# Kernel tuning notes

Measured on AMD Instinct MI355X. Metric: run time of the kernel, lower is better.

Reference implementation:

```python
import jax, jax.numpy as jnp
import numpy as np

B, S, D = 4, 1024, 1024
H, DK, DV = 16, 64, 64
EPS = 1e-5

def setup_inputs() -> dict:
    key = jax.random.key(0)
    ks = jax.random.split(key, 13)
    sc = lambda n: 1.0 / np.sqrt(n)
    return {
        "Q": jax.random.normal(ks[0], (B, S, D), jnp.float32),
        "K": jax.random.normal(ks[1], (B, S, D), jnp.float32),
        "V": jax.random.normal(ks[2], (B, S, D), jnp.float32),
        "Wq": jax.random.normal(ks[3], (D, H * DK), jnp.float32) * sc(D),
        "bq": jax.random.normal(ks[4], (H * DK,), jnp.float32) * 0.01,
        "Wk": jax.random.normal(ks[5], (D, H * DK), jnp.float32) * sc(D),
        "bk": jax.random.normal(ks[6], (H * DK,), jnp.float32) * 0.01,
        "Wv": jax.random.normal(ks[7], (D, H * DV), jnp.float32) * sc(D),
        "bv": jax.random.normal(ks[8], (H * DV,), jnp.float32) * 0.01,
        "Wo": jax.random.normal(ks[9], (H * DV, D), jnp.float32) * sc(H * DV),
        "bo": jax.random.normal(ks[10], (D,), jnp.float32) * 0.01,
        "pos_k": jax.random.normal(ks[11], (H * S, DK), jnp.float32) * 0.02,
        "pos_v": jax.random.normal(ks[12], (H * S, DV), jnp.float32) * 0.02,
        "gamma": jnp.ones((D,), jnp.float32),
        "beta": jnp.zeros((D,), jnp.float32),
    }

def reference(Q, K, V, Wq, bq, Wk, bk, Wv, bv, Wo, bo, pos_k, pos_v, gamma, beta):
    b = Q.shape[0]
    # projections + head split: [b, h, s, dk/dv]
    q = (Q @ Wq + bq).reshape(b, S, H, DK).transpose(0, 2, 1, 3)
    k = (K @ Wk + bk).reshape(b, S, H, DK).transpose(0, 2, 1, 3)
    v = (V @ Wv + bv).reshape(b, S, H, DV).transpose(0, 2, 1, 3)
    # pos_ids = arange(H*S).view(1, H, S) -> embedding lookup is just a reshape
    K_pos = pos_k.reshape(1, H, S, DK)
    V_pos = pos_v.reshape(1, H, S, DV)
    scores = jnp.einsum("bhqd,bhkd->bhqk", q, k + K_pos) / np.sqrt(DK).astype(np.float32)
    attn = jax.nn.softmax(scores, axis=-1)
    context = jnp.einsum("bhqk,bhkd->bhqd", attn, v + V_pos)
    context = context.transpose(0, 2, 1, 3).reshape(b, S, H * DV)
    out = context @ Wo + bo + Q  # residual
    mu = jnp.mean(out, axis=-1, keepdims=True)
    var = jnp.var(out, axis=-1, keepdims=True)
    out = (out - mu) * jax.lax.rsqrt(var + EPS) * gamma + beta
    return (out, attn)
```

## Files before the change

### kernel.cpp

```cpp
#include <hip/hip_runtime.h>
#include <cstdint>
#include <cstddef>


typedef __attribute__((ext_vector_type(8))) short short8;
typedef __attribute__((ext_vector_type(4))) short short4v;
typedef __attribute__((ext_vector_type(4))) float f32x4;

typedef __attribute__((address_space(1))) void gl_void;
typedef __attribute__((address_space(3))) void lds_void;

#define MFMA16(a, b, c) __builtin_amdgcn_mfma_f32_16x16x32_bf16(a, b, c, 0, 0, 0)

__device__ __forceinline__ unsigned short f2bf(float f) {
  union { float f; unsigned u; } v; v.f = f;
  unsigned r = v.u + 0x7FFFu + ((v.u >> 16) & 1u);
  return (unsigned short)(r >> 16);
}
__device__ __forceinline__ float bf2f(unsigned short h) {
  union { unsigned u; float f; } v; v.u = ((unsigned)h) << 16;
  return v.f;
}

__global__ __launch_bounds__(256) void transpose_w(
    const float* __restrict__ wq, const float* __restrict__ wk,
    const float* __restrict__ wv, const float* __restrict__ wo,
    unsigned short* __restrict__ wt) {
  __shared__ unsigned short tile[64][68];
  const int z = blockIdx.z;
  const float* W = (z == 0) ? wq : (z == 1) ? wk : (z == 2) ? wv : wo;
  unsigned short* out = wt + (size_t)z * 1048576;
  const int n0 = blockIdx.x * 64, k0 = blockIdx.y * 64;
  const int tr = threadIdx.x >> 4;
  const int tc = (threadIdx.x & 15) * 4;
#pragma unroll
  for (int i = 0; i < 4; ++i) {
    int k = tr + i * 16;
    float4 x = *reinterpret_cast<const float4*>(W + (size_t)(k0 + k) * 1024 + n0 + tc);
    tile[k][tc + 0] = f2bf(x.x); tile[k][tc + 1] = f2bf(x.y);
    tile[k][tc + 2] = f2bf(x.z); tile[k][tc + 3] = f2bf(x.w);
  }
  __syncthreads();
#pragma unroll
  for (int i = 0; i < 4; ++i) {
    int n = tr + i * 16;
    short4v o;
    o[0] = (short)tile[tc + 0][n]; o[1] = (short)tile[tc + 1][n];
    o[2] = (short)tile[tc + 2][n]; o[3] = (short)tile[tc + 3][n];
    *reinterpret_cast<short4v*>(out + (size_t)(n0 + n) * 1024 + k0 + tc) = o;
  }
}

__global__ __launch_bounds__(256) void gemm_qkv(
    const float* __restrict__ Qf, const float* __restrict__ Kf,
    const float* __restrict__ Vf, const unsigned short* __restrict__ wt,
    const float* __restrict__ bq, const float* __restrict__ bk,
    const float* __restrict__ bv, const float* __restrict__ pos_k,
    const float* __restrict__ pos_v, unsigned short* __restrict__ qb,
    unsigned short* __restrict__ kbuf, unsigned short* __restrict__ vT) {
  __shared__ unsigned short lds[8192];
  const int z = blockIdx.z;
  const float* A = (z == 0) ? Qf : (z == 1) ? Kf : Vf;
  const unsigned short* Bt = wt + (size_t)z * 1048576;
  const float* bias = (z == 0) ? bq : (z == 1) ? bk : bv;

  const int tid = threadIdx.x;
  const int lane = tid & 63;
  const int w = tid >> 6;
  const int g = lane >> 4;
  const int lr = lane & 15;
  const int wg = blockIdx.y * 8 + blockIdx.x;
  const int lg = (wg & 7) * 32 + (wg >> 3);
  const int m0 = (lg >> 3) << 7;
  const int n0 = (lg & 7) << 7;
  const int wm = w >> 1, wn = w & 1;

  const int ra0 = tid >> 2, ca = tid & 3;
  const int ra1 = ra0 + 64;
  const int wA0 = ra0 * 64 + ((ca ^ ((ra0 >> 1) & 3)) << 4);
  const int wA1 = ra1 * 64 + ((ca ^ ((ra1 >> 1) & 3)) << 4);
  const float* a0p = A + (size_t)(m0 + ra0) * 1024 + ca * 8;
  const float* a1p = A + (size_t)(m0 + ra1) * 1024 + ca * 8;

  const int c0 = (w << 6) + lane;
  const int r0 = c0 >> 2;
  const int sl0 = (c0 & 3) ^ ((r0 >> 1) & 3);
  const int c1 = c0 + 256;
  const int r1 = c1 >> 2;
  const int sl1 = (c1 & 3) ^ ((r1 >> 1) & 3);
  const size_t gb0 = ((size_t)(n0 + r0) << 10) + (sl0 << 3);
  const size_t gb1 = ((size_t)(n0 + r1) << 10) + (sl1 << 3);
  char* ldsc = (char*)lds;
  lds_void* dstB0 = (lds_void*)(ldsc + 8192 + (w << 10));
  lds_void* dstB1 = (lds_void*)(ldsc + 12288 + (w << 10));

  int offA[4], offB[4];
#pragma unroll
  for (int i = 0; i < 4; ++i) {
    int rt = (wm << 6) + (i << 4) + lr;
    offA[i] = rt * 64 + ((g ^ ((rt >> 1) & 3)) << 4);
    int nt = (wn << 6) + (i << 4) + lr;
    offB[i] = 8192 + nt * 64 + ((g ^ ((nt >> 1) & 3)) << 4);
  }

  f32x4 acc[4][4] = {};

  for (int kt = 0; kt < 32; ++kt) {
    const int kb32 = kt << 5;
    __builtin_amdgcn_global_load_lds((gl_void*)(Bt + gb0 + kb32), dstB0, 16, 0, 0);
    __builtin_amdgcn_global_load_lds((gl_void*)(Bt + gb1 + kb32), dstB1, 16, 0, 0);
    const float4 fa = *reinterpret_cast<const float4*>(a0p + kb32);
    const float4 fb = *reinterpret_cast<const float4*>(a0p + kb32 + 4);
    const float4 fc = *reinterpret_cast<const float4*>(a1p + kb32);
    const float4 fd = *reinterpret_cast<const float4*>(a1p + kb32 + 4);
    short8 pa, pb;
    pa[0] = (short)f2bf(fa.x); pa[1] = (short)f2bf(fa.y);
    pa[2] = (short)f2bf(fa.z); pa[3] = (short)f2bf(fa.w);
    pa[4] = (short)f2bf(fb.x); pa[5] = (short)f2bf(fb.y);
    pa[6] = (short)f2bf(fb.z); pa[7] = (short)f2bf(fb.w);
    pb[0] = (short)f2bf(fc.x); pb[1] = (short)f2bf(fc.y);
    pb[2] = (short)f2bf(fc.z); pb[3] = (short)f2bf(fc.w);
    pb[4] = (short)f2bf(fd.x); pb[5] = (short)f2bf(fd.y);
    pb[6] = (short)f2bf(fd.z); pb[7] = (short)f2bf(fd.w);
    *reinterpret_cast<short8*>(ldsc + wA0) = pa;
    *reinterpret_cast<short8*>(ldsc + wA1) = pb;
    __syncthreads();
    short8 am[4], bn[4];
#pragma unroll
    for (int i = 0; i < 4; ++i) {
      am[i] = *reinterpret_cast<const short8*>(ldsc + offA[i]);
      bn[i] = *reinterpret_cast<const short8*>(ldsc + offB[i]);
    }
#pragma unroll
    for (int i = 0; i < 4; ++i)
#pragma unroll
      for (int j = 0; j < 4; ++j)
        acc[i][j] = MFMA16(am[i], bn[j], acc[i][j]);
    __syncthreads();
  }

#pragma unroll
  for (int i = 0; i < 4; ++i) {
#pragma unroll
    for (int j = 0; j < 4; ++j) {
      const int n = n0 + (wn << 6) + (j << 4) + lr;
      const int hh = n >> 6, dk = n & 63;
      const float bs = bias[n];
      const int mb = m0 + (wm << 6) + (i << 4) + (g << 2);
      const int b = mb >> 10, s0 = mb & 1023;
      if (z == 2) {
        short4v o;
#pragma unroll
        for (int r = 0; r < 4; ++r) {
          const float val = acc[i][j][r] + bs +
                            pos_v[((((size_t)hh << 10) + s0 + r) << 6) + dk];
          o[r] = (short)f2bf(val);
        }
        *reinterpret_cast<short4v*>(
            vT + ((size_t)((b * 16 + hh) * 64 + dk) << 10) + s0) = o;
      } else {
#pragma unroll
        for (int r = 0; r < 4; ++r) {
          float val = acc[i][j][r];
          if (z == 0) {
            val = (val + bs) * 0.125f;
          } else {
            val = val + bs + pos_k[((((size_t)hh << 10) + s0 + r) << 6) + dk];
          }
          unsigned short* dst = (z == 0) ? qb : kbuf;
          dst[((((size_t)(b * 16 + hh) << 10) + s0 + r) << 6) + dk] = f2bf(val);
        }
      }
    }
  }
}

__global__ __launch_bounds__(256) void rowsum_kernel(
    const unsigned short* __restrict__ qb,
    const unsigned short* __restrict__ kb,
    float* __restrict__ l_out) {
  __shared__ char smem[16384];
  const int tid = threadIdx.x;
  const int lane = tid & 63;
  const int w = tid >> 6;
  const int g = lane >> 4;
  const int lr = lane & 15;
  const int wg = ((blockIdx.x & 7) << 7) + (blockIdx.x >> 3);
  const int bh = wg >> 4, qt = wg & 15;
  const int qrow0 = (qt << 6) + (w << 4);
  const size_t headoff = (size_t)bh << 16;

  const size_t qoff = headoff + (size_t)(qrow0 + lr) * 64 + (g << 3);
  const short8 a0 = *reinterpret_cast<const short8*>(qb + qoff);
  const short8 a1 = *reinterpret_cast<const short8*>(qb + qoff + 32);

  const int key0 = tid >> 3, sl0 = (tid & 7) ^ (key0 & 7);
  const int key1 = 32 + (tid >> 3), sl1 = (tid & 7) ^ (key1 & 7);
  const unsigned short* src0 = kb + headoff + (size_t)key0 * 64 + (sl0 << 3);
  const unsigned short* src1 = kb + headoff + (size_t)key1 * 64 + (sl1 << 3);

  float l[4] = {0.f, 0.f, 0.f, 0.f};
  for (int ct = 0; ct < 16; ++ct) {
    const int bo = (ct & 1) << 13;
    const int koff = ct << 12;
    __builtin_amdgcn_global_load_lds((gl_void*)(src0 + koff),
                                     (lds_void*)(smem + bo + (w << 10)), 16, 0, 0);
    __builtin_amdgcn_global_load_lds((gl_void*)(src1 + koff),
                                     (lds_void*)(smem + bo + 4096 + (w << 10)), 16, 0, 0);
    __syncthreads();
    const char* kl = smem + bo;
#pragma unroll
    for (int kf = 0; kf < 4; ++kf) {
      const int kr = (kf << 4) + lr;
      const char* row = kl + (kr << 7);
      const short8 b0 = *reinterpret_cast<const short8*>(row + ((g ^ (kr & 7)) << 4));
      const short8 b1 = *reinterpret_cast<const short8*>(row + (((4 + g) ^ (kr & 7)) << 4));
      f32x4 acc = {0.f, 0.f, 0.f, 0.f};
      acc = MFMA16(a0, b0, acc);
      acc = MFMA16(a1, b1, acc);
#pragma unroll
      for (int r = 0; r < 4; ++r) l[r] += __expf(acc[r]);
    }
  }
#pragma unroll
  for (int r = 0; r < 4; ++r) {
    l[r] += __shfl_xor(l[r], 1);
    l[r] += __shfl_xor(l[r], 2);
    l[r] += __shfl_xor(l[r], 4);
    l[r] += __shfl_xor(l[r], 8);
  }
  if (lr == 0) {
#pragma unroll
    for (int r = 0; r < 4; ++r)
      l_out[((size_t)bh << 10) + qrow0 + (g << 2) + r] = l[r];
  }
}

__global__ __launch_bounds__(256) void attn_pv_kernel(
    const unsigned short* __restrict__ qb,
    const unsigned short* __restrict__ kb,
    const unsigned short* __restrict__ vT,
    const float* __restrict__ l_in,
    unsigned short* __restrict__ ctxb,
    float* __restrict__ attn_out) {
  __shared__ char smem[40960];
  const int tid = threadIdx.x;
  const int lane = tid & 63;
  const int w = tid >> 6;
  const int g = lane >> 4;
  const int lr = lane & 15;
  const int wg = ((blockIdx.x & 7) << 7) + (blockIdx.x >> 3);
  const int bh = wg >> 4, qt = wg & 15;
  const int b = bh >> 4, h = bh & 15;
  const int qrow0 = (qt << 6) + (w << 4);
  const size_t headoff = (size_t)bh << 16;

  const size_t qoff = headoff + (size_t)(qrow0 + lr) * 64 + (g << 3);
  const short8 a0 = *reinterpret_cast<const short8*>(qb + qoff);
  const short8 a1 = *reinterpret_cast<const short8*>(qb + qoff + 32);

  float inv[4];
#pragma unroll
  for (int r = 0; r < 4; ++r)
    inv[r] = 1.0f / l_in[((size_t)bh << 10) + qrow0 + (g << 2) + r];

  const int key0 = tid >> 3, sl0 = (tid & 7) ^ (key0 & 7);
  const int key1 = 32 + (tid >> 3), sl1 = (tid & 7) ^ (key1 & 7);
  const unsigned short* ks0 = kb + headoff + (size_t)key0 * 64 + (sl0 << 3);
  const unsigned short* ks1 = kb + headoff + (size_t)key1 * 64 + (sl1 << 3);
  const unsigned short* vs0 = vT + headoff + ((size_t)key0 << 10) + (sl0 << 3);
  const unsigned short* vs1 = vT + headoff + ((size_t)key1 << 10) + (sl1 << 3);

  char* ew = smem + 32768 + (w << 11);
  float* ab = attn_out + ((size_t)bh << 20);
  f32x4 ctx[4] = {};

  for (int ct = 0; ct < 16; ++ct) {
    const int bo = (ct & 1) << 13;
    const int kc0 = ct << 6;
    __builtin_amdgcn_global_load_lds((gl_void*)(ks0 + ((size_t)kc0 << 6)),
                                     (lds_void*)(smem + bo + (w << 10)), 16, 0, 0);
    __builtin_amdgcn_global_load_lds((gl_void*)(ks1 + ((size_t)kc0 << 6)),
                                     (lds_void*)(smem + bo + 4096 + (w << 10)), 16, 0, 0);
    __builtin_amdgcn_global_load_lds((gl_void*)(vs0 + kc0),
                                     (lds_void*)(smem + 16384 + bo + (w << 10)), 16, 0, 0);
    __builtin_amdgcn_global_load_lds((gl_void*)(vs1 + kc0),
                                     (lds_void*)(smem + 16384 + bo + 4096 + (w << 10)), 16, 0, 0);
    __syncthreads();
    const char* kl = smem + bo;
    const char* vl = smem + 16384 + bo;

#pragma unroll
    for (int kf = 0; kf < 4; ++kf) {
      const int kr = (kf << 4) + lr;
      const char* row = kl + (kr << 7);
      const short8 b0 = *reinterpret_cast<const short8*>(row + ((g ^ (kr & 7)) << 4));
      const short8 b1 = *reinterpret_cast<const short8*>(row + (((4 + g) ^ (kr & 7)) << 4));
      f32x4 acc = {0.f, 0.f, 0.f, 0.f};
      acc = MFMA16(a0, b0, acc);
      acc = MFMA16(a1, b1, acc);
#pragma unroll
      for (int r = 0; r < 4; ++r) {
        const float p = __expf(acc[r]) * inv[r];
        const int prow = (g << 2) + r;
        const int kc = (kf << 4) + lr;
        *(unsigned short*)(ew + (prow << 7) + ((((kc >> 3) ^ (prow & 7))) << 4) +
                           ((kc & 7) << 1)) = f2bf(p);
      }
    }

#pragma unroll
    for (int p2 = 0; p2 < 2; ++p2) {
      const int row = lane >> 2;
      const int s = (lane & 3) + (p2 << 2);
      const short8 pv = *reinterpret_cast<const short8*>(
          ew + (row << 7) + ((s ^ (row & 7)) << 4));
      float* dst = ab + ((size_t)(qrow0 + row) << 10) + kc0 + (s << 3);
      float4 o0, o1;
      o0.x = bf2f((unsigned short)pv[0]); o0.y = bf2f((unsigned short)pv[1]);
      o0.z = bf2f((unsigned short)pv[2]); o0.w = bf2f((unsigned short)pv[3]);
      o1.x = bf2f((unsigned short)pv[4]); o1.y = bf2f((unsigned short)pv[5]);
      o1.z = bf2f((unsigned short)pv[6]); o1.w = bf2f((unsigned short)pv[7]);
      *reinterpret_cast<float4*>(dst) = o0;
      *reinterpret_cast<float4*>(dst + 4) = o1;
    }

    const short8 pa0 = *reinterpret_cast<const short8*>(
        ew + (lr << 7) + ((g ^ (lr & 7)) << 4));
    const short8 pa1 = *reinterpret_cast<const short8*>(
        ew + (lr << 7) + (((4 + g) ^ (lr & 7)) << 4));
#pragma unroll
    for (int dt = 0; dt < 4; ++dt) {
      const int dv = (dt << 4) + lr;
      const char* vrow = vl + (dv << 7);
      const short8 v0 = *reinterpret_cast<const short8*>(vrow + ((g ^ (dv & 7)) << 4));
      const short8 v1 = *reinterpret_cast<const short8*>(vrow + (((4 + g) ^ (dv & 7)) << 4));
      ctx[dt] = MFMA16(pa0, v0, ctx[dt]);
      ctx[dt] = MFMA16(pa1, v1, ctx[dt]);
    }
  }

#pragma unroll
  for (int dt = 0; dt < 4; ++dt) {
#pragma unroll
    for (int r = 0; r < 4; ++r) {
      const int srow = qrow0 + (g << 2) + r;
      const int n = (h << 6) + (dt << 4) + lr;
      ctxb[((((size_t)(b << 10)) + srow) << 10) + n] = f2bf(ctx[dt][r]);
    }
  }
}

__global__ __launch_bounds__(256) void gemm_out(
    const unsigned short* __restrict__ A, const unsigned short* __restrict__ Bt,
    const float* __restrict__ bias, const float* __restrict__ resid,
    float* __restrict__ outf) {
  __shared__ unsigned short lds[8192];
  const int tid = threadIdx.x;
  const int lane = tid & 63;
  const int w = tid >> 6;
  const int g = lane >> 4;
  const int lr = lane & 15;
  const int wg = blockIdx.y * 8 + blockIdx.x;
  const int lg = (wg & 7) * 32 + (wg >> 3);
  const int m0 = (lg >> 3) << 7;
  const int n0 = (lg & 7) << 7;
  const int wm = w >> 1, wn = w & 1;

  const int c0 = (w << 6) + lane;
  const int r0 = c0 >> 2;
  const int sl0 = (c0 & 3) ^ ((r0 >> 1) & 3);
  const int c1 = c0 + 256;
  const int r1 = c1 >> 2;
  const int sl1 = (c1 & 3) ^ ((r1 >> 1) & 3);

  const size_t ga0 = ((size_t)(m0 + r0) << 10) + (sl0 << 3);
  const size_t ga1 = ((size_t)(m0 + r1) << 10) + (sl1 << 3);
  const size_t gb0 = ((size_t)(n0 + r0) << 10) + (sl0 << 3);
  const size_t gb1 = ((size_t)(n0 + r1) << 10) + (sl1 << 3);

  char* ldsc = (char*)lds;
  lds_void* dstA0 = (lds_void*)(ldsc + (w << 10));
  lds_void* dstA1 = (lds_void*)(ldsc + 4096 + (w << 10));
  lds_void* dstB0 = (lds_void*)(ldsc + 8192 + (w << 10));
  lds_void* dstB1 = (lds_void*)(ldsc + 12288 + (w << 10));

  int offA[4], offB[4];
#pragma unroll
  for (int i = 0; i < 4; ++i) {
    int rt = (wm << 6) + (i << 4) + lr;
    offA[i] = rt * 64 + ((g ^ ((rt >> 1) & 3)) << 4);
    int nt = (wn << 6) + (i << 4) + lr;
    offB[i] = 8192 + nt * 64 + ((g ^ ((nt >> 1) & 3)) << 4);
  }

  f32x4 acc[4][4] = {};
  for (int kt = 0; kt < 32; ++kt) {
    const int kb32 = kt << 5;
    __builtin_amdgcn_global_load_lds((gl_void*)(A + ga0 + kb32), dstA0, 16, 0, 0);
    __builtin_amdgcn_global_load_lds((gl_void*)(A + ga1 + kb32), dstA1, 16, 0, 0);
    __builtin_amdgcn_global_load_lds((gl_void*)(Bt + gb0 + kb32), dstB0, 16, 0, 0);
    __builtin_amdgcn_global_load_lds((gl_void*)(Bt + gb1 + kb32), dstB1, 16, 0, 0);
    __syncthreads();
    short8 am[4], bn[4];
#pragma unroll
    for (int i = 0; i < 4; ++i) {
      am[i] = *reinterpret_cast<const short8*>(ldsc + offA[i]);
      bn[i] = *reinterpret_cast<const short8*>(ldsc + offB[i]);
    }
#pragma unroll
    for (int i = 0; i < 4; ++i)
#pragma unroll
      for (int j = 0; j < 4; ++j)
        acc[i][j] = MFMA16(am[i], bn[j], acc[i][j]);
    __syncthreads();
  }

#pragma unroll
  for (int i = 0; i < 4; ++i) {
#pragma unroll
    for (int j = 0; j < 4; ++j) {
      const int n = n0 + (wn << 6) + (j << 4) + lr;
      const float bs = bias[n];
#pragma unroll
      for (int r = 0; r < 4; ++r) {
        const int m = m0 + (wm << 6) + (i << 4) + (g << 2) + r;
        outf[((size_t)m << 10) + n] =
            acc[i][j][r] + bs + resid[((size_t)m << 10) + n];
      }
    }
  }
}

__global__ __launch_bounds__(256) void layernorm_kernel(
    const float* __restrict__ x, const float* __restrict__ gamma,
    const float* __restrict__ beta, float* __restrict__ out) {
  __shared__ float red[8];
  const int row = blockIdx.x, t = threadIdx.x;
  const float4 v = *reinterpret_cast<const float4*>(x + ((size_t)row << 10) + t * 4);
  float s1 = v.x + v.y + v.z + v.w;
  float s2 = v.x * v.x + v.y * v.y + v.z * v.z + v.w * v.w;
#pragma unroll
  for (int off = 1; off < 64; off <<= 1) {
    s1 += __shfl_xor(s1, off);
    s2 += __shfl_xor(s2, off);
  }
  const int w = t >> 6;
  if ((t & 63) == 0) { red[w * 2] = s1; red[w * 2 + 1] = s2; }
  __syncthreads();
  s1 = red[0] + red[2] + red[4] + red[6];
  s2 = red[1] + red[3] + red[5] + red[7];
  const float mu = s1 * (1.0f / 1024.0f);
  const float var = s2 * (1.0f / 1024.0f) - mu * mu;
  const float rs = rsqrtf(var + 1e-5f);
  const float4 gm = *reinterpret_cast<const float4*>(gamma + t * 4);
  const float4 bt = *reinterpret_cast<const float4*>(beta + t * 4);
  float4 o;
  o.x = (v.x - mu) * rs * gm.x + bt.x;
  o.y = (v.y - mu) * rs * gm.y + bt.y;
  o.z = (v.z - mu) * rs * gm.z + bt.z;
  o.w = (v.w - mu) * rs * gm.w + bt.w;
  *reinterpret_cast<float4*>(out + ((size_t)row << 10) + t * 4) = o;
}

static constexpr size_t OFF_QB = 0;
static constexpr size_t OFF_KB = 8388608;
static constexpr size_t OFF_VT = 16777216;
static constexpr size_t OFF_WT = 25165824;
static constexpr size_t OFF_CTX = 33554432;
static constexpr size_t OFF_LN = 41943040;
static constexpr size_t OFF_L = 58720256;

extern "C" void kernel_launch(void* const* d_in, const int* in_sizes, int n_in,
                              void* d_out, int out_size, void* d_ws, size_t ws_size,
                              hipStream_t stream) {
  (void)in_sizes; (void)n_in; (void)out_size; (void)ws_size;
  const float* Q = (const float*)d_in[0];
  const float* K = (const float*)d_in[1];
  const float* V = (const float*)d_in[2];
  const float* Wq = (const float*)d_in[3];
  const float* bq = (const float*)d_in[4];
  const float* Wk = (const float*)d_in[5];
  const float* bk = (const float*)d_in[6];
  const float* Wv = (const float*)d_in[7];
  const float* bv = (const float*)d_in[8];
  const float* Wo = (const float*)d_in[9];
  const float* bo = (const float*)d_in[10];
  const float* pos_k = (const float*)d_in[11];
  const float* pos_v = (const float*)d_in[12];
  const float* gamma = (const float*)d_in[13];
  const float* beta = (const float*)d_in[14];

  char* ws = (char*)d_ws;
  unsigned short* qb = (unsigned short*)(ws + OFF_QB);
  unsigned short* kb = (unsigned short*)(ws + OFF_KB);
  unsigned short* vT = (unsigned short*)(ws + OFF_VT);
  unsigned short* wt = (unsigned short*)(ws + OFF_WT);
  unsigned short* ctxb = (unsigned short*)(ws + OFF_CTX);
  float* lnb = (float*)(ws + OFF_LN);
  float* lbuf = (float*)(ws + OFF_L);

  float* outF = (float*)d_out;
  float* attnF = outF + 4194304;

  transpose_w<<<dim3(16, 16, 4), 256, 0, stream>>>(Wq, Wk, Wv, Wo, wt);
  gemm_qkv<<<dim3(8, 32, 3), 256, 0, stream>>>(Q, K, V, wt, bq, bk, bv,
                                               pos_k, pos_v, qb, kb, vT);
  rowsum_kernel<<<dim3(1024), 256, 0, stream>>>(qb, kb, lbuf);
  attn_pv_kernel<<<dim3(1024), 256, 0, stream>>>(qb, kb, vT, lbuf, ctxb, attnF);
  gemm_out<<<dim3(8, 32), 256, 0, stream>>>(ctxb, wt + 3145728, bo, Q, lnb);
  layernorm_kernel<<<4096, 256, 0, stream>>>(lnb, gamma, beta, outF);
}
```

Before: 227.6 us.

## Double-buffer LDS tiles to prefetch next K-step across GEMM and attention kernels

Converts the QKV projection, output projection and both attention passes to a double-buffered scheme. The next tile's global-to-LDS loads (and fp32-to-bf16 conversion of the A operand) are issued before computing on the current buffer, with one barrier per iteration instead of two. This is meant to hide global memory latency behind MFMA work. It doubles LDS use in the GEMMs, which may reduce occupancy, and relies on the async LDS loads being complete by the end-of-iteration barrier.

```diff
diff --git a/kernel.cpp b/kernel.cpp
--- a/kernel.cpp
+++ b/kernel.cpp
@@ -58,7 +58,7 @@
     const float* __restrict__ bv, const float* __restrict__ pos_k,
     const float* __restrict__ pos_v, unsigned short* __restrict__ qb,
     unsigned short* __restrict__ kbuf, unsigned short* __restrict__ vT) {
-  __shared__ unsigned short lds[8192];
+  __shared__ unsigned short lds[16384];
   const int z = blockIdx.z;
   const float* A = (z == 0) ? Qf : (z == 1) ? Kf : Vf;
   const unsigned short* Bt = wt + (size_t)z * 1048576;
@@ -91,8 +91,6 @@
   const size_t gb0 = ((size_t)(n0 + r0) << 10) + (sl0 << 3);
   const size_t gb1 = ((size_t)(n0 + r1) << 10) + (sl1 << 3);
   char* ldsc = (char*)lds;
-  lds_void* dstB0 = (lds_void*)(ldsc + 8192 + (w << 10));
-  lds_void* dstB1 = (lds_void*)(ldsc + 12288 + (w << 10));
 
   int offA[4], offB[4];
 #pragma unroll
@@ -100,19 +98,16 @@
     int rt = (wm << 6) + (i << 4) + lr;
     offA[i] = rt * 64 + ((g ^ ((rt >> 1) & 3)) << 4);
     int nt = (wn << 6) + (i << 4) + lr;
-    offB[i] = 8192 + nt * 64 + ((g ^ ((nt >> 1) & 3)) << 4);
+    offB[i] = nt * 64 + ((g ^ ((nt >> 1) & 3)) << 4);
   }
 
   f32x4 acc[4][4] = {};
 
-  for (int kt = 0; kt < 32; ++kt) {
-    const int kb32 = kt << 5;
-    __builtin_amdgcn_global_load_lds((gl_void*)(Bt + gb0 + kb32), dstB0, 16, 0, 0);
-    __builtin_amdgcn_global_load_lds((gl_void*)(Bt + gb1 + kb32), dstB1, 16, 0, 0);
-    const float4 fa = *reinterpret_cast<const float4*>(a0p + kb32);
-    const float4 fb = *reinterpret_cast<const float4*>(a0p + kb32 + 4);
-    const float4 fc = *reinterpret_cast<const float4*>(a1p + kb32);
-    const float4 fd = *reinterpret_cast<const float4*>(a1p + kb32 + 4);
+  {
+    const float4 fa = *reinterpret_cast<const float4*>(a0p);
+    const float4 fb = *reinterpret_cast<const float4*>(a0p + 4);
+    const float4 fc = *reinterpret_cast<const float4*>(a1p);
+    const float4 fd = *reinterpret_cast<const float4*>(a1p + 4);
     short8 pa, pb;
     pa[0] = (short)f2bf(fa.x); pa[1] = (short)f2bf(fa.y);
     pa[2] = (short)f2bf(fa.z); pa[3] = (short)f2bf(fa.w);
@@ -124,18 +119,52 @@
     pb[6] = (short)f2bf(fd.z); pb[7] = (short)f2bf(fd.w);
     *reinterpret_cast<short8*>(ldsc + wA0) = pa;
     *reinterpret_cast<short8*>(ldsc + wA1) = pb;
+    __builtin_amdgcn_global_load_lds((gl_void*)(Bt + gb0),
+                                     (lds_void*)(ldsc + 16384 + (w << 10)), 16, 0, 0);
+    __builtin_amdgcn_global_load_lds((gl_void*)(Bt + gb1),
+                                     (lds_void*)(ldsc + 16384 + 4096 + (w << 10)), 16, 0, 0);
     __syncthreads();
+  }
+
+  for (int kt = 0; kt < 32; ++kt) {
+    const int cur = (kt & 1) << 13;
+    const int nxt = ((kt + 1) & 1) << 13;
+    float4 fa, fb, fc, fd;
+    if (kt < 31) {
+      const int kb32 = (kt + 1) << 5;
+      __builtin_amdgcn_global_load_lds((gl_void*)(Bt + gb0 + kb32),
+                                       (lds_void*)(ldsc + 16384 + nxt + (w << 10)), 16, 0, 0);
+      __builtin_amdgcn_global_load_lds((gl_void*)(Bt + gb1 + kb32),
+                                       (lds_void*)(ldsc + 16384 + nxt + 4096 + (w << 10)), 16, 0, 0);
+      fa = *reinterpret_cast<const float4*>(a0p + kb32);
+      fb = *reinterpret_cast<const float4*>(a0p + kb32 + 4);
+      fc = *reinterpret_cast<const float4*>(a1p + kb32);
+      fd = *reinterpret_cast<const float4*>(a1p + kb32 + 4);
+    }
     short8 am[4], bn[4];
 #pragma unroll
     for (int i = 0; i < 4; ++i) {
-      am[i] = *reinterpret_cast<const short8*>(ldsc + offA[i]);
-      bn[i] = *reinterpret_cast<const short8*>(ldsc + offB[i]);
+      am[i] = *reinterpret_cast<const short8*>(ldsc + cur + offA[i]);
+      bn[i] = *reinterpret_cast<const short8*>(ldsc + 16384 + cur + offB[i]);
     }
 #pragma unroll
     for (int i = 0; i < 4; ++i)
 #pragma unroll
       for (int j = 0; j < 4; ++j)
         acc[i][j] = MFMA16(am[i], bn[j], acc[i][j]);
+    if (kt < 31) {
+      short8 pa, pb;
+      pa[0] = (short)f2bf(fa.x); pa[1] = (short)f2bf(fa.y);
+      pa[2] = (short)f2bf(fa.z); pa[3] = (short)f2bf(fa.w);
+      pa[4] = (short)f2bf(fb.x); pa[5] = (short)f2bf(fb.y);
+      pa[6] = (short)f2bf(fb.z); pa[7] = (short)f2bf(fb.w);
+      pb[0] = (short)f2bf(fc.x); pb[1] = (short)f2bf(fc.y);
+      pb[2] = (short)f2bf(fc.z); pb[3] = (short)f2bf(fc.w);
+      pb[4] = (short)f2bf(fd.x); pb[5] = (short)f2bf(fd.y);
+      pb[6] = (short)f2bf(fd.z); pb[7] = (short)f2bf(fd.w);
+      *reinterpret_cast<short8*>(ldsc + nxt + wA0) = pa;
+      *reinterpret_cast<short8*>(ldsc + nxt + wA1) = pb;
+    }
     __syncthreads();
   }
 
@@ -199,16 +228,24 @@
   const unsigned short* src0 = kb + headoff + (size_t)key0 * 64 + (sl0 << 3);
   const unsigned short* src1 = kb + headoff + (size_t)key1 * 64 + (sl1 << 3);
 
+  __builtin_amdgcn_global_load_lds((gl_void*)src0,
+                                   (lds_void*)(smem + (w << 10)), 16, 0, 0);
+  __builtin_amdgcn_global_load_lds((gl_void*)src1,
+                                   (lds_void*)(smem + 4096 + (w << 10)), 16, 0, 0);
+  __syncthreads();
+
   float l[4] = {0.f, 0.f, 0.f, 0.f};
   for (int ct = 0; ct < 16; ++ct) {
-    const int bo = (ct & 1) << 13;
-    const int koff = ct << 12;
-    __builtin_amdgcn_global_load_lds((gl_void*)(src0 + koff),
-                                     (lds_void*)(smem + bo + (w << 10)), 16, 0, 0);
-    __builtin_amdgcn_global_load_lds((gl_void*)(src1 + koff),
-                                     (lds_void*)(smem + bo + 4096 + (w << 10)), 16, 0, 0);
-    __syncthreads();
-    const char* kl = smem + bo;
+    const int cur = (ct & 1) << 13;
+    if (ct < 15) {
+      const int nxt = ((ct + 1) & 1) << 13;
+      const int koff = (ct + 1) << 12;
+      __builtin_amdgcn_global_load_lds((gl_void*)(src0 + koff),
+                                       (lds_void*)(smem + nxt + (w << 10)), 16, 0, 0);
+      __builtin_amdgcn_global_load_lds((gl_void*)(src1 + koff),
+                                       (lds_void*)(smem + nxt + 4096 + (w << 10)), 16, 0, 0);
+    }
+    const char* kl = smem + cur;
 #pragma unroll
     for (int kf = 0; kf < 4; ++kf) {
       const int kr = (kf << 4) + lr;
@@ -221,6 +258,7 @@
 #pragma unroll
       for (int r = 0; r < 4; ++r) l[r] += __expf(acc[r]);
     }
+    __syncthreads();
   }
 #pragma unroll
   for (int r = 0; r < 4; ++r) {
@@ -275,20 +313,33 @@
   float* ab = attn_out + ((size_t)bh << 20);
   f32x4 ctx[4] = {};
 
+  __builtin_amdgcn_global_load_lds((gl_void*)ks0,
+                                   (lds_void*)(smem + (w << 10)), 16, 0, 0);
+  __builtin_amdgcn_global_load_lds((gl_void*)ks1,
+                                   (lds_void*)(smem + 4096 + (w << 10)), 16, 0, 0);
+  __builtin_amdgcn_global_load_lds((gl_void*)vs0,
+                                   (lds_void*)(smem + 16384 + (w << 10)), 16, 0, 0);
+  __builtin_amdgcn_global_load_lds((gl_void*)vs1,
+                                   (lds_void*)(smem + 16384 + 4096 + (w << 10)), 16, 0, 0);
+  __syncthreads();
+
   for (int ct = 0; ct < 16; ++ct) {
-    const int bo = (ct & 1) << 13;
+    const int cur = (ct & 1) << 13;
     const int kc0 = ct << 6;
-    __builtin_amdgcn_global_load_lds((gl_void*)(ks0 + ((size_t)kc0 << 6)),
-                                     (lds_void*)(smem + bo + (w << 10)), 16, 0, 0);
-    __builtin_amdgcn_global_load_lds((gl_void*)(ks1 + ((size_t)kc0 << 6)),
-                                     (lds_void*)(smem + bo + 4096 + (w << 10)), 16, 0, 0);
-    __builtin_amdgcn_global_load_lds((gl_void*)(vs0 + kc0),
-                                     (lds_void*)(smem + 16384 + bo + (w << 10)), 16, 0, 0);
-    __builtin_amdgcn_global_load_lds((gl_void*)(vs1 + kc0),
-                                     (lds_void*)(smem + 16384 + bo + 4096 + (w << 10)), 16, 0, 0);
-    __syncthreads();
-    const char* kl = smem + bo;
-    const char* vl = smem + 16384 + bo;
+    if (ct < 15) {
+      const int nxt = ((ct + 1) & 1) << 13;
+      const int kn = (ct + 1) << 6;
+      __builtin_amdgcn_global_load_lds((gl_void*)(ks0 + ((size_t)kn << 6)),
+                                       (lds_void*)(smem + nxt + (w << 10)), 16, 0, 0);
+      __builtin_amdgcn_global_load_lds((gl_void*)(ks1 + ((size_t)kn << 6)),
+                                       (lds_void*)(smem + nxt + 4096 + (w << 10)), 16, 0, 0);
+      __builtin_amdgcn_global_load_lds((gl_void*)(vs0 + kn),
+                                       (lds_void*)(smem + 16384 + nxt + (w << 10)), 16, 0, 0);
+      __builtin_amdgcn_global_load_lds((gl_void*)(vs1 + kn),
+                                       (lds_void*)(smem + 16384 + nxt + 4096 + (w << 10)), 16, 0, 0);
+    }
+    const char* kl = smem + cur;
+    const char* vl = smem + 16384 + cur;
 
 #pragma unroll
     for (int kf = 0; kf < 4; ++kf) {
@@ -338,6 +389,7 @@
       ctx[dt] = MFMA16(pa0, v0, ctx[dt]);
       ctx[dt] = MFMA16(pa1, v1, ctx[dt]);
     }
+    __syncthreads();
   }
 
 #pragma unroll
@@ -355,7 +407,7 @@
     const unsigned short* __restrict__ A, const unsigned short* __restrict__ Bt,
     const float* __restrict__ bias, const float* __restrict__ resid,
     float* __restrict__ outf) {
-  __shared__ unsigned short lds[8192];
+  __shared__ unsigned short lds[16384];
   const int tid = threadIdx.x;
   const int lane = tid & 63;
   const int w = tid >> 6;
@@ -380,10 +432,6 @@
   const size_t gb1 = ((size_t)(n0 + r1) << 10) + (sl1 << 3);
 
   char* ldsc = (char*)lds;
-  lds_void* dstA0 = (lds_void*)(ldsc + (w << 10));
-  lds_void* dstA1 = (lds_void*)(ldsc + 4096 + (w << 10));
-  lds_void* dstB0 = (lds_void*)(ldsc + 8192 + (w << 10));
-  lds_void* dstB1 = (lds_void*)(ldsc + 12288 + (w << 10));
 
   int offA[4], offB[4];
 #pragma unroll
@@ -391,22 +439,39 @@
     int rt = (wm << 6) + (i << 4) + lr;
     offA[i] = rt * 64 + ((g ^ ((rt >> 1) & 3)) << 4);
     int nt = (wn << 6) + (i << 4) + lr;
-    offB[i] = 8192 + nt * 64 + ((g ^ ((nt >> 1) & 3)) << 4);
-  }
+    offB[i] = nt * 64 + ((g ^ ((nt >> 1) & 3)) << 4);
+  }
+
+  __builtin_amdgcn_global_load_lds((gl_void*)(A + ga0),
+                                   (lds_void*)(ldsc + (w << 10)), 16, 0, 0);
+  __builtin_amdgcn_global_load_lds((gl_void*)(A + ga1),
+                                   (lds_void*)(ldsc + 4096 + (w << 10)), 16, 0, 0);
+  __builtin_amdgcn_global_load_lds((gl_void*)(Bt + gb0),
+                                   (lds_void*)(ldsc + 16384 + (w << 10)), 16, 0, 0);
+  __builtin_amdgcn_global_load_lds((gl_void*)(Bt + gb1),
+                                   (lds_void*)(ldsc + 16384 + 4096 + (w << 10)), 16, 0, 0);
+  __syncthreads();
 
   f32x4 acc[4][4] = {};
   for (int kt = 0; kt < 32; ++kt) {
-    const int kb32 = kt << 5;
-    __builtin_amdgcn_global_load_lds((gl_void*)(A + ga0 + kb32), dstA0, 16, 0, 0);
-    __builtin_amdgcn_global_load_lds((gl_void*)(A + ga1 + kb32), dstA1, 16, 0, 0);
-    __builtin_amdgcn_global_load_lds((gl_void*)(Bt + gb0 + kb32), dstB0, 16, 0, 0);
-    __builtin_amdgcn_global_load_lds((gl_void*)(Bt + gb1 + kb32), dstB1, 16, 0, 0);
-    __syncthreads();
+    const int cur = (kt & 1) << 13;
+    if (kt < 31) {
+      const int nxt = ((kt + 1) & 1) << 13;
+      const int kb32 = (kt + 1) << 5;
+      __builtin_amdgcn_global_load_lds((gl_void*)(A + ga0 + kb32),
+                                       (lds_void*)(ldsc + nxt + (w << 10)), 16, 0, 0);
+      __builtin_amdgcn_global_load_lds((gl_void*)(A + ga1 + kb32),
+                                       (lds_void*)(ldsc + nxt + 4096 + (w << 10)), 16, 0, 0);
+      __builtin_amdgcn_global_load_lds((gl_void*)(Bt + gb0 + kb32),
+                                       (lds_void*)(ldsc + 16384 + nxt + (w << 10)), 16, 0, 0);
+      __builtin_amdgcn_global_load_lds((gl_void*)(Bt + gb1 + kb32),
+                                       (lds_void*)(ldsc + 16384 + nxt + 4096 + (w << 10)), 16, 0, 0);
+    }
     short8 am[4], bn[4];
 #pragma unroll
     for (int i = 0; i < 4; ++i) {
-      am[i] = *reinterpret_cast<const short8*>(ldsc + offA[i]);
-      bn[i] = *reinterpret_cast<const short8*>(ldsc + offB[i]);
+      am[i] = *reinterpret_cast<const short8*>(ldsc + cur + offA[i]);
+      bn[i] = *reinterpret_cast<const short8*>(ldsc + 16384 + cur + offB[i]);
     }
 #pragma unroll
     for (int i = 0; i < 4; ++i)
```

After: 204.3 us. 10.2% less time.
